# Kernel tuning notes

Measured on AMD Instinct MI355X. Metric: run time of the kernel, lower is better.

The kernel has to match this reference:

```python
import jax, jax.numpy as jnp
import numpy as np

DIM = 1024
N_HEADS = 16
HEAD_DIM = DIM // N_HEADS
LN_EPS = 1e-5


def layer_norm(x, gamma, beta, eps=LN_EPS):
    mu = jnp.mean(x, axis=-1, keepdims=True)
    var = jnp.var(x, axis=-1, keepdims=True)
    return (x - mu) * jax.lax.rsqrt(var + eps) * gamma + beta


def setup_inputs() -> dict:
    key = jax.random.key(0)
    ks = jax.random.split(key, 12)
    B, Nq, Nc, D = 2, 1024, 4096, DIM
    s = 1.0 / np.sqrt(D)  # torch Linear default init scale (uniform bound)
    inp = {
        "query": jax.random.normal(ks[0], (B, Nq, D), jnp.float32),
        "context": jax.random.normal(ks[1], (B, Nc, D), jnp.float32),
        "wq": jax.random.uniform(ks[2], (D, D), jnp.float32, -s, s),
        "bq": jax.random.uniform(ks[3], (D,), jnp.float32, -s, s),
        "wk": jax.random.uniform(ks[4], (D, D), jnp.float32, -s, s),
        "bk": jax.random.uniform(ks[5], (D,), jnp.float32, -s, s),
        "wv": jax.random.uniform(ks[6], (D, D), jnp.float32, -s, s),
        "bv": jax.random.uniform(ks[7], (D,), jnp.float32, -s, s),
        "wo": jax.random.uniform(ks[8], (D, D), jnp.float32, -s, s),
        "bo": jax.random.uniform(ks[9], (D,), jnp.float32, -s, s),
        "g_q": jnp.ones((D,), jnp.float32),
        "b_q": jnp.zeros((D,), jnp.float32),
        "g_kv": jnp.ones((D,), jnp.float32),
        "b_kv": jnp.zeros((D,), jnp.float32),
    }
    return inp


def reference(query, context, wq, bq, wk, bk, wv, bv, wo, bo, g_q, b_q, g_kv, b_kv):
    B, Nq, D = query.shape
    Nc = context.shape[1]
    H, Hd = N_HEADS, HEAD_DIM

    qn = layer_norm(query, g_q, b_q)        # [B,Nq,D]
    cn = layer_norm(context, g_kv, b_kv)    # [B,Nc,D]

    # torch Linear: y = x @ W.T + b; weights here stored as [out,in]
    Q = (jnp.einsum('bnd,ed->bne', qn, wq) + bq).reshape(B, Nq, H, Hd)
    K = (jnp.einsum('bnd,ed->bne', cn, wk) + bk).reshape(B, Nc, H, Hd)
    V = (jnp.einsum('bnd,ed->bne', cn, wv) + bv).reshape(B, Nc, H, Hd)

    scale = 1.0 / np.sqrt(Hd)
    scores = jnp.einsum('bqhd,bkhd->bhqk', Q, K) * scale  # [B,H,Nq,Nc]
    attn = jax.nn.softmax(scores, axis=-1)
    out = jnp.einsum('bhqk,bkhd->bqhd', attn, V).reshape(B, Nq, D)

    return qn + (jnp.einsum('bnd,ed->bne', out, wo) + bo)
```

## Files before the change

kernel.cpp:

```cpp
#include <hip/hip_runtime.h>

typedef unsigned short u16;
typedef __attribute__((ext_vector_type(8))) __bf16 bf16x8;
typedef __attribute__((ext_vector_type(4))) float f32x4;

struct alignas(8) U16x4 { u16 x, y, z, w; };

__device__ __forceinline__ u16 f2bf(float f) {
    union { float f; unsigned u; } v; v.f = f;
    unsigned r = v.u + 0x7fffu + ((v.u >> 16) & 1u);
    return (u16)(r >> 16);
}

__device__ __forceinline__ unsigned cvt_pk_bf16(float lo, float hi) {
    unsigned r;
    asm("v_cvt_pk_bf16_f32 %0, %1, %2" : "=v"(r) : "v"(lo), "v"(hi));
    return r;
}

__device__ __forceinline__ float fexp2(float x) {
    float r;
    asm("v_exp_f32 %0, %1" : "=v"(r) : "v"(x));
    return r;
}

__device__ __forceinline__ void gload_lds16(const void* g, void* l) {
    __builtin_amdgcn_global_load_lds(
        (__attribute__((address_space(1))) void*)g,
        (__attribute__((address_space(3))) void*)l, 16, 0, 0);
}

__global__ __launch_bounds__(256)
void ln_fused(const float* __restrict__ x, const float* __restrict__ g,
              const float* __restrict__ be, float* __restrict__ y32,
              u16* __restrict__ y16)
{
    const int wid = threadIdx.x >> 6, lane = threadIdx.x & 63;
    const size_t row = (size_t)blockIdx.x * 4 + wid;
    const float4* xr = (const float4*)(x + row * 1024);
    float4 v[4];
    float s = 0.f, ss = 0.f;
#pragma unroll
    for (int i = 0; i < 4; ++i) {
        v[i] = xr[i * 64 + lane];
        s  += (v[i].x + v[i].y) + (v[i].z + v[i].w);
        ss += (v[i].x * v[i].x + v[i].y * v[i].y) + (v[i].z * v[i].z + v[i].w * v[i].w);
    }
#pragma unroll
    for (int o = 32; o; o >>= 1) { s += __shfl_xor(s, o, 64); ss += __shfl_xor(ss, o, 64); }
    const float mu = s * (1.f / 1024.f);
    const float rstd = rsqrtf(ss * (1.f / 1024.f) - mu * mu + 1e-5f);
#pragma unroll
    for (int i = 0; i < 4; ++i) {
        float4 gv = ((const float4*)g)[i * 64 + lane];
        float4 bv = ((const float4*)be)[i * 64 + lane];
        float4 o;
        o.x = (v[i].x - mu) * rstd * gv.x + bv.x;
        o.y = (v[i].y - mu) * rstd * gv.y + bv.y;
        o.z = (v[i].z - mu) * rstd * gv.z + bv.z;
        o.w = (v[i].w - mu) * rstd * gv.w + bv.w;
        if (y32) ((float4*)(y32 + row * 1024))[i * 64 + lane] = o;
        U16x4 pk = { f2bf(o.x), f2bf(o.y), f2bf(o.z), f2bf(o.w) };
        ((U16x4*)(y16 + row * 1024))[i * 64 + lane] = pk;
    }
}

__global__ __launch_bounds__(256)
void wconv4(const float4* __restrict__ a, const float4* __restrict__ b,
            const float4* __restrict__ c, const float4* __restrict__ d,
            U16x4* __restrict__ oa, U16x4* __restrict__ ob,
            U16x4* __restrict__ oc, U16x4* __restrict__ od)
{
    const int i = blockIdx.x * 256 + threadIdx.x;
    float4 v;
    v = a[i]; oa[i] = { f2bf(v.x), f2bf(v.y), f2bf(v.z), f2bf(v.w) };
    v = b[i]; ob[i] = { f2bf(v.x), f2bf(v.y), f2bf(v.z), f2bf(v.w) };
    v = c[i]; oc[i] = { f2bf(v.x), f2bf(v.y), f2bf(v.z), f2bf(v.w) };
    v = d[i]; od[i] = { f2bf(v.x), f2bf(v.y), f2bf(v.z), f2bf(v.w) };
}

__global__ __launch_bounds__(512, 4)
void gemm_kv(const u16* __restrict__ A, const u16* __restrict__ Wk,
             const u16* __restrict__ Wv, const float* __restrict__ bkp,
             const float* __restrict__ bvp, u16* __restrict__ Kout,
             u16* __restrict__ Vt)
{
    constexpr int K = 1024, N = 1024, BK = 64;
    __shared__ __align__(16) u16 sA[128 * BK];
    __shared__ __align__(16) u16 sK[128 * BK];
    __shared__ __align__(16) u16 sV[128 * BK];
    const int tid = threadIdx.x, wid = tid >> 6, lane = tid & 63;
    const int lr = lane & 15, lg = lane >> 4;
    const int wr = wid >> 2, wc = wid & 3;
    const int row0 = blockIdx.x * 128, col0 = blockIdx.y * 128;
    const int srow = wid * 8 + (lane >> 3), scol = (lane & 7) * 8;

    const u16* Ag = A  + (size_t)(row0 + srow) * K + scol;
    const u16* Kg = Wk + (size_t)(col0 + srow) * K + scol;
    const u16* Vg = Wv + (size_t)(col0 + srow) * K + scol;

    f32x4 ka[4][2], va[4][2];
#pragma unroll
    for (int m = 0; m < 4; ++m)
#pragma unroll
        for (int n = 0; n < 2; ++n) {
            ka[m][n] = (f32x4){0.f, 0.f, 0.f, 0.f};
            va[m][n] = (f32x4){0.f, 0.f, 0.f, 0.f};
        }

    for (int k0 = 0; k0 < K; k0 += BK) {
        __syncthreads();
#pragma unroll
        for (int i = 0; i < 2; ++i) {
            gload_lds16(Ag + (size_t)i * 64 * K + k0, (char*)sA + i * 8192 + wid * 1024);
            gload_lds16(Kg + (size_t)i * 64 * K + k0, (char*)sK + i * 8192 + wid * 1024);
            gload_lds16(Vg + (size_t)i * 64 * K + k0, (char*)sV + i * 8192 + wid * 1024);
        }
        __syncthreads();
#pragma unroll
        for (int kk = 0; kk < 2; ++kk) {
            bf16x8 af[4], bk[2], bv[2];
#pragma unroll
            for (int m = 0; m < 4; ++m)
                af[m] = *(const bf16x8*)&sA[(wr * 64 + m * 16 + lr) * BK + kk * 32 + lg * 8];
#pragma unroll
            for (int n = 0; n < 2; ++n) {
                bk[n] = *(const bf16x8*)&sK[(wc * 32 + n * 16 + lr) * BK + kk * 32 + lg * 8];
                bv[n] = *(const bf16x8*)&sV[(wc * 32 + n * 16 + lr) * BK + kk * 32 + lg * 8];
            }
#pragma unroll
            for (int m = 0; m < 4; ++m)
#pragma unroll
                for (int n = 0; n < 2; ++n) {
                    ka[m][n] = __builtin_amdgcn_mfma_f32_16x16x32_bf16(af[m], bk[n], ka[m][n], 0, 0, 0);
                    va[m][n] = __builtin_amdgcn_mfma_f32_16x16x32_bf16(af[m], bv[n], va[m][n], 0, 0, 0);
                }
        }
    }

#pragma unroll
    for (int m = 0; m < 4; ++m) {
#pragma unroll
        for (int n = 0; n < 2; ++n) {
            const int r = row0 + wr * 64 + m * 16 + lg * 4;
            const int c = col0 + wc * 32 + n * 16 + lr;
            const float kb = bkp[c], vb = bvp[c];
#pragma unroll
            for (int j = 0; j < 4; ++j)
                Kout[(size_t)(r + j) * N + c] = f2bf(ka[m][n][j] + kb);
            const size_t base = ((size_t)(r >> 12) * 1024 + c) * 4096 + (r & 4095);
            U16x4 pk = { f2bf(va[m][n][0] + vb), f2bf(va[m][n][1] + vb),
                         f2bf(va[m][n][2] + vb), f2bf(va[m][n][3] + vb) };
            *(U16x4*)&Vt[base] = pk;
        }
    }
}

template<int MODE>
__global__ __launch_bounds__(256)
void gemm_bt64(const u16* __restrict__ A, const u16* __restrict__ W,
               const float* __restrict__ bias, const float* __restrict__ resid,
               void* __restrict__ Cp, int M, int N, int K, float alpha)
{
    constexpr int BK = 64;
    __shared__ __align__(16) u16 sA[64 * BK];
    __shared__ __align__(16) u16 sB[128 * BK];
    const int tid = threadIdx.x, wid = tid >> 6, lane = tid & 63;
    const int lr = lane & 15, lg = lane >> 4;
    const int wr = wid >> 1, wc = wid & 1;
    const int row0 = blockIdx.x * 64, col0 = blockIdx.y * 128;
    const int srow = wid * 8 + (lane >> 3), scol = (lane & 7) * 8;

    const u16* Ag = A + (size_t)(row0 + srow) * K + scol;
    const u16* Wg = W + (size_t)(col0 + srow) * K + scol;

    f32x4 acc[2][4];
#pragma unroll
    for (int m = 0; m < 2; ++m)
#pragma unroll
        for (int n = 0; n < 4; ++n) acc[m][n] = (f32x4){0.f, 0.f, 0.f, 0.f};

    for (int k0 = 0; k0 < K; k0 += BK) {
        __syncthreads();
#pragma unroll
        for (int i = 0; i < 2; ++i)
            gload_lds16(Ag + (size_t)i * 32 * K + k0, (char*)sA + i * 4096 + wid * 1024);
#pragma unroll
        for (int i = 0; i < 4; ++i)
            gload_lds16(Wg + (size_t)i * 32 * K + k0, (char*)sB + i * 4096 + wid * 1024);
        __syncthreads();
#pragma unroll
        for (int kk = 0; kk < 2; ++kk) {
            bf16x8 af[2], bfr[4];
#pragma unroll
            for (int m = 0; m < 2; ++m)
                af[m] = *(const bf16x8*)&sA[(wr * 32 + m * 16 + lr) * BK + kk * 32 + lg * 8];
#pragma unroll
            for (int n = 0; n < 4; ++n)
                bfr[n] = *(const bf16x8*)&sB[(wc * 64 + n * 16 + lr) * BK + kk * 32 + lg * 8];
#pragma unroll
            for (int m = 0; m < 2; ++m)
#pragma unroll
                for (int n = 0; n < 4; ++n)
                    acc[m][n] = __builtin_amdgcn_mfma_f32_16x16x32_bf16(af[m], bfr[n], acc[m][n], 0, 0, 0);
        }
    }

#pragma unroll
    for (int m = 0; m < 2; ++m) {
#pragma unroll
        for (int n = 0; n < 4; ++n) {
            const int r = row0 + wr * 32 + m * 16 + lg * 4;
            const int c = col0 + wc * 64 + n * 16 + lr;
            const float bv = bias[c];
            if constexpr (MODE == 0) {
                u16* C = (u16*)Cp;
#pragma unroll
                for (int j = 0; j < 4; ++j)
                    C[(size_t)(r + j) * N + c] = f2bf((acc[m][n][j] + bv) * alpha);
            } else {
                float* C = (float*)Cp;
#pragma unroll
                for (int j = 0; j < 4; ++j)
                    C[(size_t)(r + j) * N + c] =
                        (acc[m][n][j] + bv) * alpha + resid[(size_t)(r + j) * N + c];
            }
        }
    }
}

__global__ __launch_bounds__(512, 4)
void attn_fwd(const u16* __restrict__ Q, const u16* __restrict__ Kg,
              const u16* __restrict__ Vt, u16* __restrict__ O)
{
    constexpr int D = 1024, CSTR = 19;
    __shared__ __align__(16) char smem[81920];

    const int tid = threadIdx.x, wid = tid >> 6, lane = tid & 63;
    const int grp = wid >> 2, w = wid & 3;
    const int lr = lane & 15, lg = lane >> 4;
    const int rs = lr & 7;
    const int pkey = (lr & 7) << 4;

    const int fid = blockIdx.x;
    const int wk = (fid & 7) * 64 + (fid >> 3);
    const int qblk = wk & 15, h = (wk >> 4) & 15, b = wk >> 8;
    const int q0 = qblk * 64 + w * 16;

    const u16* Qrow = Q + (size_t)(b * 1024 + q0 + lr) * D + h * 64;
    const bf16x8 qf0 = *(const bf16x8*)(Qrow + lg * 8);
    const bf16x8 qf1 = *(const bf16x8*)(Qrow + 32 + lg * 8);

    const int srow = w * 8 + (lane >> 3);
    const int scol = ((lane & 7) ^ (srow & 7)) * 8;
    const u16* kp = Kg + (size_t)(b * 4096 + grp * 2048 + srow) * D + h * 64 + scol;
    const u16* vp = Vt + ((size_t)(b * 16 + h) * 64 + srow) * 4096 + grp * 2048 + scol;

    char* sProw = smem + 65536 + wid * 2048 + lr * 128;

    f32x4 po[4];
#pragma unroll
    for (int df = 0; df < 4; ++df) po[df] = (f32x4){0.f, 0.f, 0.f, 0.f};
    float m = -INFINITY, l = 0.f;

    {
        char* kd = smem + grp * 8192 + w * 1024;
        char* vd = smem + 32768 + grp * 8192 + w * 1024;
        gload_lds16(kp,                      kd);
        gload_lds16(kp + (size_t)32 * D,     kd + 4096);
        gload_lds16(vp,                      vd);
        gload_lds16(vp + (size_t)32 * 4096,  vd + 4096);
        kp += (size_t)64 * D; vp += 64;
    }
    asm volatile("s_waitcnt vmcnt(0)" ::: "memory");
    asm volatile("s_barrier" ::: "memory");

    for (int t = 0; t < 32; ++t) {
        const int cur = t & 1;
        if (t < 31) {
            char* kd = smem + (cur ^ 1) * 16384 + grp * 8192 + w * 1024;
            char* vd = smem + 32768 + (cur ^ 1) * 16384 + grp * 8192 + w * 1024;
            gload_lds16(kp,                      kd);
            gload_lds16(kp + (size_t)32 * D,     kd + 4096);
            gload_lds16(vp,                      vd);
            gload_lds16(vp + (size_t)32 * 4096,  vd + 4096);
            kp += (size_t)64 * D; vp += 64;
        }

        const u16* kb = (const u16*)(smem + cur * 16384 + grp * 8192);
        const u16* vb = (const u16*)(smem + 32768 + cur * 16384 + grp * 8192);

        f32x4 s4[4];
#pragma unroll
        for (int f = 0; f < 4; ++f) {
            const int r = f * 16 + lr;
            bf16x8 k0v = *(const bf16x8*)&kb[r * 64 + (lg ^ rs) * 8];
            bf16x8 k1v = *(const bf16x8*)&kb[r * 64 + ((lg + 4) ^ rs) * 8];
            f32x4 z = (f32x4){0.f, 0.f, 0.f, 0.f};
            z = __builtin_amdgcn_mfma_f32_16x16x32_bf16(k0v, qf0, z, 0, 0, 0);
            s4[f] = __builtin_amdgcn_mfma_f32_16x16x32_bf16(k1v, qf1, z, 0, 0, 0);
        }

        float pmax = fmaxf(fmaxf(fmaxf(s4[0][0], s4[0][1]), fmaxf(s4[0][2], s4[0][3])),
                     fmaxf(fmaxf(fmaxf(s4[1][0], s4[1][1]), fmaxf(s4[1][2], s4[1][3])),
                     fmaxf(fmaxf(fmaxf(s4[2][0], s4[2][1]), fmaxf(s4[2][2], s4[2][3])),
                           fmaxf(fmaxf(s4[3][0], s4[3][1]), fmaxf(s4[3][2], s4[3][3])))));
        if (!__all(pmax <= m)) {
            float tmax = fmaxf(pmax, __shfl_xor(pmax, 16, 64));
            tmax = fmaxf(tmax, __shfl_xor(tmax, 32, 64));
            const float mn = fmaxf(m, tmax);
            const float corr = fexp2(m - mn);
            l *= corr;
#pragma unroll
            for (int df = 0; df < 4; ++df) po[df] *= corr;
            m = mn;
        }
        float lsum = 0.f;
        uint2 pk[4];
#pragma unroll
        for (int f = 0; f < 4; ++f) {
            float p0 = fexp2(s4[f][0] - m);
            float p1 = fexp2(s4[f][1] - m);
            float p2 = fexp2(s4[f][2] - m);
            float p3 = fexp2(s4[f][3] - m);
            lsum += (p0 + p1) + (p2 + p3);
            pk[f].x = cvt_pk_bf16(p0, p1);
            pk[f].y = cvt_pk_bf16(p2, p3);
        }
        l += lsum;

#pragma unroll
        for (int f = 0; f < 4; ++f)
            *(uint2*)(sProw + ((f * 32 + lg * 8) ^ pkey)) = pk[f];

#pragma unroll
        for (int c = 0; c < 2; ++c) {
            bf16x8 pf = *(const bf16x8*)(sProw + ((c * 64 + lg * 16) ^ pkey));
#pragma unroll
            for (int df = 0; df < 4; ++df) {
                const int r = df * 16 + lr;
                bf16x8 vf = *(const bf16x8*)&vb[r * 64 + ((c * 4 + lg) ^ rs) * 8];
                po[df] = __builtin_amdgcn_mfma_f32_16x16x32_bf16(vf, pf, po[df], 0, 0, 0);
            }
        }

        asm volatile("s_waitcnt vmcnt(0)" ::: "memory");
        asm volatile("s_barrier" ::: "memory");
    }

    l += __shfl_xor(l, 16, 64);
    l += __shfl_xor(l, 32, 64);

    float* cb = (float*)smem;
    if (grp == 1) {
        float* dst = cb + (size_t)(w * 64 + lane) * CSTR;
        dst[0] = m; dst[1] = l;
#pragma unroll
        for (int df = 0; df < 4; ++df)
#pragma unroll
            for (int j = 0; j < 4; ++j) dst[2 + df * 4 + j] = po[df][j];
    }
    __syncthreads();
    if (grp == 0) {
        const float* src = cb + (size_t)(w * 64 + lane) * CSTR;
        const float m1 = src[0], l1 = src[1];
        const float M = fmaxf(m, m1);
        const float c0 = fexp2(m - M), c1 = fexp2(m1 - M);
        const float rl = 1.f / (l * c0 + l1 * c1);
        u16* Orow = O + (size_t)(b * 1024 + q0 + lr) * D + h * 64;
#pragma unroll
        for (int df = 0; df < 4; ++df) {
            U16x4 opk = { f2bf((po[df][0] * c0 + src[2 + df * 4 + 0] * c1) * rl),
                          f2bf((po[df][1] * c0 + src[2 + df * 4 + 1] * c1) * rl),
                          f2bf((po[df][2] * c0 + src[2 + df * 4 + 2] * c1) * rl),
                          f2bf((po[df][3] * c0 + src[2 + df * 4 + 3] * c1) * rl) };
            *(U16x4*)&Orow[df * 16 + lg * 4] = opk;
        }
    }
}

extern "C" void kernel_launch(void* const* d_in, const int* in_sizes, int n_in,
                              void* d_out, int out_size, void* d_ws, size_t ws_size,
                              hipStream_t stream)
{
    const float* query   = (const float*)d_in[0];
    const float* context = (const float*)d_in[1];
    const float* wq = (const float*)d_in[2];
    const float* bq = (const float*)d_in[3];
    const float* wk = (const float*)d_in[4];
    const float* bk = (const float*)d_in[5];
    const float* wv = (const float*)d_in[6];
    const float* bv = (const float*)d_in[7];
    const float* wo = (const float*)d_in[8];
    const float* bo = (const float*)d_in[9];
    const float* g_q  = (const float*)d_in[10];
    const float* b_q  = (const float*)d_in[11];
    const float* g_kv = (const float*)d_in[12];
    const float* b_kv = (const float*)d_in[13];

    char* p = (char*)d_ws;
    auto alloc = [&](size_t bytes) { char* r = p; p += (bytes + 255) & ~(size_t)255; return r; };
    u16*   wqb  = (u16*)alloc(1024 * 1024 * 2);
    u16*   wkb  = (u16*)alloc(1024 * 1024 * 2);
    u16*   wvb  = (u16*)alloc(1024 * 1024 * 2);
    u16*   wob  = (u16*)alloc(1024 * 1024 * 2);
    float* qn32 = (float*)alloc((size_t)2048 * 1024 * 4);
    u16*   qnb  = (u16*)alloc((size_t)2048 * 1024 * 2);
    u16*   cnb  = (u16*)alloc((size_t)8192 * 1024 * 2);
    u16*   Qb   = (u16*)alloc((size_t)2048 * 1024 * 2);
    u16*   Kb   = (u16*)alloc((size_t)8192 * 1024 * 2);
    u16*   Vtb  = (u16*)alloc((size_t)8192 * 1024 * 2);
    u16*   AOb  = (u16*)alloc((size_t)2048 * 1024 * 2);

    wconv4<<<1024, 256, 0, stream>>>((const float4*)wq, (const float4*)wk,
                                     (const float4*)wv, (const float4*)wo,
                                     (U16x4*)wqb, (U16x4*)wkb, (U16x4*)wvb, (U16x4*)wob);
    ln_fused<<<512, 256, 0, stream>>>(query, g_q, b_q, qn32, qnb);
    ln_fused<<<2048, 256, 0, stream>>>(context, g_kv, b_kv, nullptr, cnb);

    gemm_bt64<0><<<dim3(32, 8), 256, 0, stream>>>(qnb, wqb, bq, nullptr, Qb, 2048, 1024, 1024, 0.18033688f);
    gemm_kv<<<dim3(64, 8), 512, 0, stream>>>(cnb, wkb, wvb, bk, bv, Kb, Vtb);

    attn_fwd<<<dim3(512), 512, 0, stream>>>(Qb, Kb, Vtb, AOb);

    gemm_bt64<1><<<dim3(32, 8), 256, 0, stream>>>(AOb, wob, bo, qn32, d_out, 2048, 1024, 1024, 1.0f);
}
```

Before: 169.3 us.

## Software-pipeline PV MFMA behind next QK tile and merge prep kernels

The attention loop now defers the P·V MFMAs of each tile to the start of the next iteration, where they run alongside the QK^T MFMAs under raised wave priority. V fragments are preloaded into registers before the barrier, and the final tile's PV is issued after the loop. The aim is to keep the matrix units busy while the softmax exp and max work proceeds. Separately, the weight conversion and both layer norms are merged into one launch to save launch overhead. The cost is more live registers for the V fragments and an extra lgkmcnt wait before each barrier.

```diff
diff --git a/kernel.cpp b/kernel.cpp
--- a/kernel.cpp
+++ b/kernel.cpp
@@ -5,6 +5,8 @@
 typedef __attribute__((ext_vector_type(4))) float f32x4;
 
 struct alignas(8) U16x4 { u16 x, y, z, w; };
+
+#define MFMA16(a, b, c) __builtin_amdgcn_mfma_f32_16x16x32_bf16(a, b, c, 0, 0, 0)
 
 __device__ __forceinline__ u16 f2bf(float f) {
     union { float f; unsigned u; } v; v.f = f;
@@ -31,52 +33,56 @@
 }
 
 __global__ __launch_bounds__(256)
-void ln_fused(const float* __restrict__ x, const float* __restrict__ g,
-              const float* __restrict__ be, float* __restrict__ y32,
-              u16* __restrict__ y16)
+void prep(const float* __restrict__ query, const float* __restrict__ context,
+          const float* __restrict__ g_q, const float* __restrict__ b_q,
+          const float* __restrict__ g_kv, const float* __restrict__ b_kv,
+          float* __restrict__ qn32, u16* __restrict__ qnb, u16* __restrict__ cnb,
+          const float4* __restrict__ w0, const float4* __restrict__ w1,
+          const float4* __restrict__ w2, const float4* __restrict__ w3,
+          U16x4* __restrict__ o0, U16x4* __restrict__ o1,
+          U16x4* __restrict__ o2, U16x4* __restrict__ o3)
 {
-    const int wid = threadIdx.x >> 6, lane = threadIdx.x & 63;
-    const size_t row = (size_t)blockIdx.x * 4 + wid;
-    const float4* xr = (const float4*)(x + row * 1024);
-    float4 v[4];
-    float s = 0.f, ss = 0.f;
-#pragma unroll
-    for (int i = 0; i < 4; ++i) {
-        v[i] = xr[i * 64 + lane];
-        s  += (v[i].x + v[i].y) + (v[i].z + v[i].w);
-        ss += (v[i].x * v[i].x + v[i].y * v[i].y) + (v[i].z * v[i].z + v[i].w * v[i].w);
-    }
-#pragma unroll
-    for (int o = 32; o; o >>= 1) { s += __shfl_xor(s, o, 64); ss += __shfl_xor(ss, o, 64); }
-    const float mu = s * (1.f / 1024.f);
-    const float rstd = rsqrtf(ss * (1.f / 1024.f) - mu * mu + 1e-5f);
-#pragma unroll
-    for (int i = 0; i < 4; ++i) {
-        float4 gv = ((const float4*)g)[i * 64 + lane];
-        float4 bv = ((const float4*)be)[i * 64 + lane];
-        float4 o;
-        o.x = (v[i].x - mu) * rstd * gv.x + bv.x;
-        o.y = (v[i].y - mu) * rstd * gv.y + bv.y;
-        o.z = (v[i].z - mu) * rstd * gv.z + bv.z;
-        o.w = (v[i].w - mu) * rstd * gv.w + bv.w;
-        if (y32) ((float4*)(y32 + row * 1024))[i * 64 + lane] = o;
-        U16x4 pk = { f2bf(o.x), f2bf(o.y), f2bf(o.z), f2bf(o.w) };
-        ((U16x4*)(y16 + row * 1024))[i * 64 + lane] = pk;
-    }
-}
-
-__global__ __launch_bounds__(256)
-void wconv4(const float4* __restrict__ a, const float4* __restrict__ b,
-            const float4* __restrict__ c, const float4* __restrict__ d,
-            U16x4* __restrict__ oa, U16x4* __restrict__ ob,
-            U16x4* __restrict__ oc, U16x4* __restrict__ od)
-{
-    const int i = blockIdx.x * 256 + threadIdx.x;
-    float4 v;
-    v = a[i]; oa[i] = { f2bf(v.x), f2bf(v.y), f2bf(v.z), f2bf(v.w) };
-    v = b[i]; ob[i] = { f2bf(v.x), f2bf(v.y), f2bf(v.z), f2bf(v.w) };
-    v = c[i]; oc[i] = { f2bf(v.x), f2bf(v.y), f2bf(v.z), f2bf(v.w) };
-    v = d[i]; od[i] = { f2bf(v.x), f2bf(v.y), f2bf(v.z), f2bf(v.w) };
+    const int blk = blockIdx.x;
+    if (blk < 2560) {
+        const float *x, *g, *be; float* y32; u16* y16; int rb;
+        if (blk < 512) { x = query;   g = g_q;  be = b_q;  y32 = qn32;    y16 = qnb; rb = blk; }
+        else           { x = context; g = g_kv; be = b_kv; y32 = nullptr; y16 = cnb; rb = blk - 512; }
+        const int wid = threadIdx.x >> 6, lane = threadIdx.x & 63;
+        const size_t row = (size_t)rb * 4 + wid;
+        const float4* xr = (const float4*)(x + row * 1024);
+        float4 v[4];
+        float s = 0.f, ss = 0.f;
+#pragma unroll
+        for (int i = 0; i < 4; ++i) {
+            v[i] = xr[i * 64 + lane];
+            s  += (v[i].x + v[i].y) + (v[i].z + v[i].w);
+            ss += (v[i].x * v[i].x + v[i].y * v[i].y) + (v[i].z * v[i].z + v[i].w * v[i].w);
+        }
+#pragma unroll
+        for (int o = 32; o; o >>= 1) { s += __shfl_xor(s, o, 64); ss += __shfl_xor(ss, o, 64); }
+        const float mu = s * (1.f / 1024.f);
+        const float rstd = rsqrtf(ss * (1.f / 1024.f) - mu * mu + 1e-5f);
+#pragma unroll
+        for (int i = 0; i < 4; ++i) {
+            float4 gv = ((const float4*)g)[i * 64 + lane];
+            float4 bv = ((const float4*)be)[i * 64 + lane];
+            float4 o;
+            o.x = (v[i].x - mu) * rstd * gv.x + bv.x;
+            o.y = (v[i].y - mu) * rstd * gv.y + bv.y;
+            o.z = (v[i].z - mu) * rstd * gv.z + bv.z;
+            o.w = (v[i].w - mu) * rstd * gv.w + bv.w;
+            if (y32) ((float4*)(y32 + row * 1024))[i * 64 + lane] = o;
+            U16x4 pk = { f2bf(o.x), f2bf(o.y), f2bf(o.z), f2bf(o.w) };
+            ((U16x4*)(y16 + row * 1024))[i * 64 + lane] = pk;
+        }
+    } else {
+        const int i = (blk - 2560) * 256 + threadIdx.x;
+        float4 v;
+        v = w0[i]; o0[i] = { f2bf(v.x), f2bf(v.y), f2bf(v.z), f2bf(v.w) };
+        v = w1[i]; o1[i] = { f2bf(v.x), f2bf(v.y), f2bf(v.z), f2bf(v.w) };
+        v = w2[i]; o2[i] = { f2bf(v.x), f2bf(v.y), f2bf(v.z), f2bf(v.w) };
+        v = w3[i]; o3[i] = { f2bf(v.x), f2bf(v.y), f2bf(v.z), f2bf(v.w) };
+    }
 }
 
 __global__ __launch_bounds__(512, 4)
@@ -132,8 +138,8 @@
             for (int m = 0; m < 4; ++m)
 #pragma unroll
                 for (int n = 0; n < 2; ++n) {
-                    ka[m][n] = __builtin_amdgcn_mfma_f32_16x16x32_bf16(af[m], bk[n], ka[m][n], 0, 0, 0);
-                    va[m][n] = __builtin_amdgcn_mfma_f32_16x16x32_bf16(af[m], bv[n], va[m][n], 0, 0, 0);
+                    ka[m][n] = MFMA16(af[m], bk[n], ka[m][n]);
+                    va[m][n] = MFMA16(af[m], bv[n], va[m][n]);
                 }
         }
     }
@@ -202,7 +208,7 @@
             for (int m = 0; m < 2; ++m)
 #pragma unroll
                 for (int n = 0; n < 4; ++n)
-                    acc[m][n] = __builtin_amdgcn_mfma_f32_16x16x32_bf16(af[m], bfr[n], acc[m][n], 0, 0, 0);
+                    acc[m][n] = MFMA16(af[m], bfr[n], acc[m][n]);
         }
     }
 
@@ -243,8 +249,8 @@
     const int pkey = (lr & 7) << 4;
 
     const int fid = blockIdx.x;
-    const int wk = (fid & 7) * 64 + (fid >> 3);
-    const int qblk = wk & 15, h = (wk >> 4) & 15, b = wk >> 8;
+    const int wkid = (fid & 7) * 64 + (fid >> 3);
+    const int qblk = wkid & 15, h = (wkid >> 4) & 15, b = wkid >> 8;
     const int q0 = qblk * 64 + w * 16;
 
     const u16* Qrow = Q + (size_t)(b * 1024 + q0 + lr) * D + h * 64;
@@ -262,6 +268,20 @@
 #pragma unroll
     for (int df = 0; df < 4; ++df) po[df] = (f32x4){0.f, 0.f, 0.f, 0.f};
     float m = -INFINITY, l = 0.f;
+    bf16x8 vr0, vr1, vr2, vr3, vr4, vr5, vr6, vr7;
+
+    auto pv_step = [&]() {
+        bf16x8 pf0 = *(const bf16x8*)(sProw + ((lg * 16) ^ pkey));
+        bf16x8 pf1 = *(const bf16x8*)(sProw + ((64 + lg * 16) ^ pkey));
+        po[0] = MFMA16(vr0, pf0, po[0]);
+        po[1] = MFMA16(vr1, pf0, po[1]);
+        po[2] = MFMA16(vr2, pf0, po[2]);
+        po[3] = MFMA16(vr3, pf0, po[3]);
+        po[0] = MFMA16(vr4, pf1, po[0]);
+        po[1] = MFMA16(vr5, pf1, po[1]);
+        po[2] = MFMA16(vr6, pf1, po[2]);
+        po[3] = MFMA16(vr7, pf1, po[3]);
+    };
 
     {
         char* kd = smem + grp * 8192 + w * 1024;
@@ -290,6 +310,9 @@
         const u16* kb = (const u16*)(smem + cur * 16384 + grp * 8192);
         const u16* vb = (const u16*)(smem + 32768 + cur * 16384 + grp * 8192);
 
+        __builtin_amdgcn_s_setprio(1);
+        if (t > 0) pv_step();
+
         f32x4 s4[4];
 #pragma unroll
         for (int f = 0; f < 4; ++f) {
@@ -297,9 +320,19 @@
             bf16x8 k0v = *(const bf16x8*)&kb[r * 64 + (lg ^ rs) * 8];
             bf16x8 k1v = *(const bf16x8*)&kb[r * 64 + ((lg + 4) ^ rs) * 8];
             f32x4 z = (f32x4){0.f, 0.f, 0.f, 0.f};
-            z = __builtin_amdgcn_mfma_f32_16x16x32_bf16(k0v, qf0, z, 0, 0, 0);
-            s4[f] = __builtin_amdgcn_mfma_f32_16x16x32_bf16(k1v, qf1, z, 0, 0, 0);
-        }
+            z = MFMA16(k0v, qf0, z);
+            s4[f] = MFMA16(k1v, qf1, z);
+        }
+        __builtin_amdgcn_s_setprio(0);
+
+        vr0 = *(const bf16x8*)&vb[(0 * 16 + lr) * 64 + ((0 + lg) ^ rs) * 8];
+        vr1 = *(const bf16x8*)&vb[(1 * 16 + lr) * 64 + ((0 + lg) ^ rs) * 8];
+        vr2 = *(const bf16x8*)&vb[(2 * 16 + lr) * 64 + ((0 + lg) ^ rs) * 8];
+        vr3 = *(const bf16x8*)&vb[(3 * 16 + lr) * 64 + ((0 + lg) ^ rs) * 8];
+        vr4 = *(const bf16x8*)&vb[(0 * 16 + lr) * 64 + ((4 + lg) ^ rs) * 8];
+        vr5 = *(const bf16x8*)&vb[(1 * 16 + lr) * 64 + ((4 + lg) ^ rs) * 8];
+        vr6 = *(const bf16x8*)&vb[(2 * 16 + lr) * 64 + ((4 + lg) ^ rs) * 8];
+        vr7 = *(const bf16x8*)&vb[(3 * 16 + lr) * 64 + ((4 + lg) ^ rs) * 8];
 
         float pmax = fmaxf(fmaxf(fmaxf(s4[0][0], s4[0][1]), fmaxf(s4[0][2], s4[0][3])),
                      fmaxf(fmaxf(fmaxf(s4[1][0], s4[1][1]), fmaxf(s4[1][2], s4[1][3])),
@@ -333,20 +366,11 @@
         for (int f = 0; f < 4; ++f)
             *(uint2*)(sProw + ((f * 32 + lg * 8) ^ pkey)) = pk[f];
 
-#pragma unroll
-        for (int c = 0; c < 2; ++c) {
-            bf16x8 pf = *(const bf16x8*)(sProw + ((c * 64 + lg * 16) ^ pkey));
-#pragma unroll
-            for (int df = 0; df < 4; ++df) {
-                const int r = df * 16 + lr;
-                bf16x8 vf = *(const bf16x8*)&vb[r * 64 + ((c * 4 + lg) ^ rs) * 8];
-                po[df] = __builtin_amdgcn_mfma_f32_16x16x32_bf16(vf, pf, po[df], 0, 0, 0);
-            }
-        }
-
-        asm volatile("s_waitcnt vmcnt(0)" ::: "memory");
+        asm volatile("s_waitcnt vmcnt(0) lgkmcnt(0)" ::: "memory");
         asm volatile("s_barrier" ::: "memory");
     }
+
+    pv_step();
 
     l += __shfl_xor(l, 16, 64);
     l += __shfl_xor(l, 32, 64);
@@ -412,11 +436,11 @@
     u16*   Vtb  = (u16*)alloc((size_t)8192 * 1024 * 2);
     u16*   AOb  = (u16*)alloc((size_t)2048 * 1024 * 2);
 
-    wconv4<<<1024, 256, 0, stream>>>((const float4*)wq, (const float4*)wk,
-                                     (const float4*)wv, (const float4*)wo,
-                                     (U16x4*)wqb, (U16x4*)wkb, (U16x4*)wvb, (U16x4*)wob);
-    ln_fused<<<512, 256, 0, stream>>>(query, g_q, b_q, qn32, qnb);
-    ln_fused<<<2048, 256, 0, stream>>>(context, g_kv, b_kv, nullptr, cnb);
+    prep<<<3584, 256, 0, stream>>>(query, context, g_q, b_q, g_kv, b_kv,
+                                   qn32, qnb, cnb,
+                                   (const float4*)wq, (const float4*)wk,
+                                   (const float4*)wv, (const float4*)wo,
+                                   (U16x4*)wqb, (U16x4*)wkb, (U16x4*)wvb, (U16x4*)wob);
 
     gemm_bt64<0><<<dim3(32, 8), 256, 0, stream>>>(qnb, wqb, bq, nullptr, Qb, 2048, 1024, 1024, 0.18033688f);
     gemm_kv<<<dim3(64, 8), 512, 0, stream>>>(cnb, wkb, wvb, bk, bv, Kb, Vtb);
```

Result: faster. 164.6 us (-2.8%).
